# Kernel optimization log

Hardware: AMD Instinct MI355X
Metric: run time of the kernel (lower is better)

The kernel has to match this reference:

```python
import jax, jax.numpy as jnp
import numpy as np

THRESHOLD = 0.5
ALPHA = 1.0
RATIO = 1.0
BACKGROUND = 0
OBJECT = 1


def cxcywh_to_xyxy(b):
    cxcy, wh = b[..., :2], b[..., 2:]
    return jnp.concatenate([cxcy - wh / 2.0, cxcy + wh / 2.0], axis=-1)


def xyxy_to_cxcywh(b):
    xy1, xy2 = b[..., :2], b[..., 2:]
    return jnp.concatenate([(xy1 + xy2) / 2.0, xy2 - xy1], axis=-1)


def cxcywh_to_gcxgcy(c, d):
    # standard SSD encoding with variances (0.1, 0.2)
    g_cxcy = (c[..., :2] - d[..., :2]) / (d[..., 2:] / 10.0)
    g_wh = jnp.log(c[..., 2:] / d[..., 2:]) * 5.0
    return jnp.concatenate([g_cxcy, g_wh], axis=-1)


def box_iou(a, b):
    # a: [M,4] xyxy, b: [A,4] xyxy -> [M,A]
    area_a = (a[:, 2] - a[:, 0]) * (a[:, 3] - a[:, 1])
    area_b = (b[:, 2] - b[:, 0]) * (b[:, 3] - b[:, 1])
    lt = jnp.maximum(a[:, None, :2], b[None, :, :2])
    rb = jnp.minimum(a[:, None, 2:], b[None, :, 2:])
    wh = jnp.clip(rb - lt, 0.0)
    inter = wh[..., 0] * wh[..., 1]
    return inter / (area_a[:, None] + area_b[None, :] - inter)


def setup_inputs() -> dict:
    B, A, M = 32, 16384, 64
    key = jax.random.key(0)
    k1, k2, k3, k4 = jax.random.split(key, 4)
    x = jax.random.normal(k1, (B, A, 4), dtype=jnp.float32)
    y = jax.random.normal(k2, (B, A, 2), dtype=jnp.float32)
    # valid xyxy GT boxes in [0,1]
    u = jax.random.uniform(k3, (B, M, 4), dtype=jnp.float32)
    xy1 = u[..., :2] * 0.7
    wh = 0.05 + u[..., 2:] * 0.25
    boxes = jnp.concatenate([xy1, xy1 + wh], axis=-1)
    # default (prior) boxes in cxcywh
    ud = jax.random.uniform(k4, (A, 4), dtype=jnp.float32)
    dcxcy = 0.05 + ud[..., :2] * 0.9
    dwh = 0.05 + ud[..., 2:] * 0.25
    default = jnp.concatenate([dcxcy, dwh], axis=-1)
    labels = jnp.ones((B, M), dtype=jnp.int32)  # all GT boxes are 'object'
    return {"x": x, "y": y, "boxes": boxes, "labels": labels, "default": default}


def reference(x, y, boxes, labels, default):
    B, A = x.shape[0], default.shape[0]
    M = boxes.shape[1]
    default_xy = cxcywh_to_xyxy(default)  # [A,4]

    def match(bx):  # bx: [M,4]
        iou = box_iou(bx, default_xy)              # [M,A]
        overlap = iou.max(axis=0)                  # [A] best GT per anchor
        digit = jnp.argmax(iou, axis=0)            # [A]
        best_anchor = jnp.argmax(iou, axis=1)      # [M] best anchor per GT
        digit = digit.at[best_anchor].set(jnp.arange(M))
        overlap = overlap.at[best_anchor].set(1.0)
        return digit, overlap

    digit, overlap = jax.vmap(match)(boxes)        # [B,A], [B,A]
    matched = jnp.take_along_axis(boxes, digit[..., None], axis=1)  # [B,A,4]
    localization = cxcywh_to_gcxgcy(xyxy_to_cxcywh(matched), default)  # [B,A,4]

    gathered = jnp.take_along_axis(labels, digit, axis=1)           # [B,A]
    classification = jnp.where(overlap < THRESHOLD, BACKGROUND, gathered)

    positives = classification == OBJECT
    total = positives.sum()
    totf = total.astype(x.dtype)

    # SmoothL1 (beta=1), mean over positive elements (P*4)
    d = x - localization
    ad = jnp.abs(d)
    sl1 = jnp.where(ad < 1.0, 0.5 * d * d, ad - 0.5)
    smooth = (sl1 * positives[..., None]).sum() / (totf * 4.0)

    # per-anchor cross entropy
    logp = jax.nn.log_softmax(y, axis=-1)                 # [B,A,2]
    ent = -jnp.take_along_axis(logp, classification[..., None], axis=-1)[..., 0]

    pos_sum = jnp.where(positives, ent, 0.0).sum()
    # hard negative mining: sort negatives descending, keep int(total*ratio)
    negv = jnp.where(positives, 0.0, ent).ravel()         # CE >= 0, so masking with 0 is safe
    neg_sorted = jnp.sort(negv)[::-1]
    keep = (totf * RATIO).astype(jnp.int32)
    neg_sum = jnp.where(jnp.arange(negv.shape[0]) < keep, neg_sorted, 0.0).sum()

    entropy = ALPHA * (pos_sum + neg_sum) / totf
    return smooth + entropy
```

## Files before the change

kernel.cpp:

```cpp
#include <hip/hip_runtime.h>

#define THRESH 0.5f

__global__ void __launch_bounds__(256) k_matchboth(
        const float* __restrict__ boxes, const float* __restrict__ dflt,
        unsigned* __restrict__ match, unsigned long long* __restrict__ bestchunk,
        unsigned* __restrict__ zerop, int B, int A, int M, int chunks) {
    __shared__ float4 bx[128];
    __shared__ float barea[128];
    __shared__ float4 anch[256];
    __shared__ float adarea[256];
    __shared__ unsigned long long lm[128];
    int tid = threadIdx.x;
    if (blockIdx.x == 0) {
        for (int j = tid; j < 4112; j += 256) zerop[j] = 0u;
    }
    int b = blockIdx.x / chunks;
    int chunk = blockIdx.x - b * chunks;
    int a = chunk * 256 + tid;
    if (tid < M) {
        float4 bv = *reinterpret_cast<const float4*>(boxes + ((size_t)b * M + tid) * 4);
        bx[tid] = bv;
        barea[tid] = (bv.z - bv.x) * (bv.w - bv.y);
        lm[tid] = 0ull;
    }
    bool aval = (a < A);
    float dx1 = 0.f, dy1 = 0.f, dx2 = 0.f, dy2 = 0.f, darea = 0.f;
    if (aval) {
        float4 dv = *reinterpret_cast<const float4*>(dflt + (size_t)a * 4);
        dx1 = dv.x - dv.z * 0.5f; dy1 = dv.y - dv.w * 0.5f;
        dx2 = dv.x + dv.z * 0.5f; dy2 = dv.y + dv.w * 0.5f;
        darea = (dx2 - dx1) * (dy2 - dy1);
    }
    anch[tid] = make_float4(dx1, dy1, dx2, dy2);
    adarea[tid] = darea;
    __syncthreads();
    if (aval) {
        float binter = -1.0f, bS = 1.0f; int bm = 0;
        #pragma unroll 4
        for (int m = 0; m < M; ++m) {
            float4 bb = bx[m];
            float lx = fmaxf(bb.x, dx1), ly = fmaxf(bb.y, dy1);
            float rx = fminf(bb.z, dx2), ry = fminf(bb.w, dy2);
            float w = fmaxf(rx - lx, 0.f), h = fmaxf(ry - ly, 0.f);
            float inter = w * h;
            float S = barea[m] + darea;
            bool gt = inter * bS > binter * S;
            binter = gt ? inter : binter;
            bS     = gt ? S : bS;
            bm     = gt ? m : bm;
        }
        unsigned fl = (3.0f * binter >= bS) ? (1u << 30) : 0u;
        match[(size_t)b * A + a] = (unsigned)bm | fl;
    }
    int wv = tid >> 6, lane = tid & 63;
    int abase = chunk * 256 + wv * 64;
    int kmax = min(64, A - abase);
    if (lane < M && kmax > 0) {
        float4 bb = bx[lane];
        float ba = barea[lane];
        float binter = -1.0f, bS = 1.0f; int bk = 0;
        #pragma unroll 4
        for (int k = 0; k < kmax; ++k) {
            float4 av = anch[wv * 64 + k];
            float lx = fmaxf(bb.x, av.x), ly = fmaxf(bb.y, av.y);
            float rx = fminf(bb.z, av.z), ry = fminf(bb.w, av.w);
            float w = fmaxf(rx - lx, 0.f), h = fmaxf(ry - ly, 0.f);
            float inter = w * h;
            float S = ba + adarea[wv * 64 + k];
            bool gt = inter * bS > binter * S;
            binter = gt ? inter : binter;
            bS     = gt ? S : bS;
            bk     = gt ? k : bk;
        }
        float best = binter / (bS - binter);
        atomicMax(&lm[lane], ((unsigned long long)__float_as_uint(best) << 32) |
                             (unsigned long long)(unsigned)(~(abase + bk)));
    }
    __syncthreads();
    if (tid < M)
        bestchunk[((size_t)b * chunks + chunk) * M + tid] = lm[tid];
}

__global__ void __launch_bounds__(256) k_main(
        const float* __restrict__ x, const float* __restrict__ y,
        const float* __restrict__ boxes, const int* __restrict__ labels,
        const float* __restrict__ dflt, const unsigned* __restrict__ match,
        const unsigned long long* __restrict__ bestchunk,
        float* __restrict__ negv, unsigned* __restrict__ hist1,
        unsigned* __restrict__ scal, int A, int M, int chunks, int N) {
    __shared__ unsigned lh[2048];
    __shared__ float4 sbx[128];
    __shared__ int slab[128];
    __shared__ int ovr[1024];
    int tid = threadIdx.x;
    for (int j = tid; j < 2048; j += 256) lh[j] = 0u;
    for (int j = tid; j < 1024; j += 256) ovr[j] = -1;
    int i0 = (blockIdx.x * 256 + tid) * 4;
    int base = blockIdx.x * 1024;
    int b = (int)(((long long)blockIdx.x * 1024) / A);
    if (tid < M) {
        sbx[tid] = *reinterpret_cast<const float4*>(boxes + ((size_t)b * M + tid) * 4);
        slab[tid] = labels[b * M + tid];
    }
    __syncthreads();
    if (tid < M) {
        unsigned long long p = 0ull;
        const unsigned long long* bp = bestchunk + (size_t)b * chunks * M + tid;
        for (int c = 0; c < chunks; ++c) {
            unsigned long long q = bp[(size_t)c * M];
            p = (q > p) ? q : p;
        }
        unsigned a = ~(unsigned)(p & 0xFFFFFFFFull);
        int target = b * A + (int)a;
        if (target >= base && target < base + 1024)
            atomicMax(&ovr[target - base], tid);
    }
    __syncthreads();
    float l_smooth = 0.f, l_pos = 0.f; int l_cnt = 0;
    if (i0 + 3 < N) {
        uint4 w4 = *reinterpret_cast<const uint4*>(match + i0);
        const float4* yp = reinterpret_cast<const float4*>(y + (size_t)i0 * 2);
        float4 ya = yp[0], yb = yp[1];
        unsigned wws[4] = {w4.x, w4.y, w4.z, w4.w};
        float y0s[4] = {ya.x, ya.z, yb.x, yb.z};
        float y1s[4] = {ya.y, ya.w, yb.y, yb.w};
        float vs[4];
        int a0 = i0 - b * A;
        #pragma unroll
        for (int e = 0; e < 4; ++e) {
            unsigned w = wws[e];
            int digit = (int)(w & 0xFFFFu);
            bool flag = (w & 0x40000000u) != 0u;
            int o = ovr[tid * 4 + e];
            if (o >= 0) { digit = o; flag = true; }
            int c = flag ? slab[digit] : 0;
            bool pos = (c == 1);
            float y0 = y0s[e], y1v = y1s[e];
            float mx = fmaxf(y0, y1v);
            float lse = mx + log1pf(expf(-fabsf(y0 - y1v)));
            float ent = lse - ((c == 0) ? y0 : y1v);
            float v = pos ? 0.f : ent;
            vs[e] = v;
            if (pos) {
                float4 bv = sbx[digit];
                float4 dv = *reinterpret_cast<const float4*>(dflt + (size_t)(a0 + e) * 4);
                float4 xv = *reinterpret_cast<const float4*>(x + (size_t)(i0 + e) * 4);
                float cw = bv.z - bv.x, ch = bv.w - bv.y;
                float ccx = (bv.x + bv.z) * 0.5f, ccy = (bv.y + bv.w) * 0.5f;
                float l0 = (ccx - dv.x) / (dv.z * 0.1f);
                float l1 = (ccy - dv.y) / (dv.w * 0.1f);
                float l2 = logf(cw / dv.z) * 5.f;
                float l3 = logf(ch / dv.w) * 5.f;
                float s = 0.f, d, ad;
                d = xv.x - l0; ad = fabsf(d); s += (ad < 1.f) ? 0.5f * d * d : ad - 0.5f;
                d = xv.y - l1; ad = fabsf(d); s += (ad < 1.f) ? 0.5f * d * d : ad - 0.5f;
                d = xv.z - l2; ad = fabsf(d); s += (ad < 1.f) ? 0.5f * d * d : ad - 0.5f;
                d = xv.w - l3; ad = fabsf(d); s += (ad < 1.f) ? 0.5f * d * d : ad - 0.5f;
                l_smooth += s; l_pos += ent; l_cnt += 1;
            }
            atomicAdd(&lh[__float_as_uint(v) >> 21], 1u);
        }
        *reinterpret_cast<float4*>(negv + i0) = make_float4(vs[0], vs[1], vs[2], vs[3]);
    }
    for (int off = 32; off > 0; off >>= 1) {
        l_smooth += __shfl_down(l_smooth, off, 64);
        l_pos    += __shfl_down(l_pos, off, 64);
        l_cnt    += __shfl_down(l_cnt, off, 64);
    }
    __shared__ float rs[4], rp[4]; __shared__ int rc[4];
    int wv = tid >> 6;
    if ((tid & 63) == 0) { rs[wv] = l_smooth; rp[wv] = l_pos; rc[wv] = l_cnt; }
    __syncthreads();
    if (tid == 0) {
        float ss = rs[0] + rs[1] + rs[2] + rs[3];
        float pp = rp[0] + rp[1] + rp[2] + rp[3];
        int   cc = rc[0] + rc[1] + rc[2] + rc[3];
        if (ss != 0.f) atomicAdd((float*)&scal[2], ss);
        if (pp != 0.f) atomicAdd((float*)&scal[1], pp);
        if (cc)        atomicAdd((int*)&scal[0], cc);
    }
    __syncthreads();
    for (int j = tid; j < 2048; j += 256) {
        unsigned h = lh[j];
        if (h) atomicAdd(&hist1[j], h);
    }
}

__device__ __forceinline__ void scan_find(const unsigned* __restrict__ hist, int nbins,
                                          unsigned k, unsigned* ts, unsigned* res) {
    int t = threadIdx.x;
    int per = nbins >> 8;
    unsigned s = 0;
    for (int j = 0; j < per; ++j) s += hist[t * per + j];
    ts[t] = s;
    __syncthreads();
    for (int off = 1; off < 256; off <<= 1) {
        unsigned add = (t >= off) ? ts[t - off] : 0u;
        __syncthreads();
        ts[t] += add;
        __syncthreads();
    }
    unsigned total = ts[255];
    unsigned P = (t == 0) ? 0u : ts[t - 1];
    for (int j = 0; j < per; ++j) {
        unsigned h = hist[t * per + j];
        P += h;
        unsigned above = total - P;
        if (above < k && k <= above + h) { res[0] = (unsigned)(t * per + j); res[1] = k - above; }
    }
    __syncthreads();
}

__global__ void __launch_bounds__(256) k_refine2(
        const float* __restrict__ negv, int N, const unsigned* __restrict__ scal,
        const unsigned* __restrict__ hist1, unsigned* __restrict__ hist2) {
    __shared__ unsigned ts[256], res[2], lh[2048];
    scan_find(hist1, 2048, scal[0], ts, res);
    unsigned bin1 = res[0];
    for (int j = threadIdx.x; j < 2048; j += 256) lh[j] = 0u;
    __syncthreads();
    for (int i = (blockIdx.x * 256 + threadIdx.x) * 4; i < N; i += gridDim.x * 1024) {
        float4 v4 = *reinterpret_cast<const float4*>(negv + i);
        unsigned u;
        u = __float_as_uint(v4.x); if ((u >> 21) == bin1) atomicAdd(&lh[(u >> 10) & 0x7FFu], 1u);
        u = __float_as_uint(v4.y); if ((u >> 21) == bin1) atomicAdd(&lh[(u >> 10) & 0x7FFu], 1u);
        u = __float_as_uint(v4.z); if ((u >> 21) == bin1) atomicAdd(&lh[(u >> 10) & 0x7FFu], 1u);
        u = __float_as_uint(v4.w); if ((u >> 21) == bin1) atomicAdd(&lh[(u >> 10) & 0x7FFu], 1u);
    }
    __syncthreads();
    for (int j = threadIdx.x; j < 2048; j += 256) {
        unsigned h = lh[j];
        if (h) atomicAdd(&hist2[j], h);
    }
}

__global__ void __launch_bounds__(256) k_sum(
        const float* __restrict__ negv, int N, unsigned* __restrict__ scal,
        const unsigned* __restrict__ hist1, const unsigned* __restrict__ hist2,
        float* __restrict__ out) {
    __shared__ unsigned ts[256], res[2];
    scan_find(hist1, 2048, scal[0], ts, res);
    unsigned bin1 = res[0], k1 = res[1];
    scan_find(hist2, 2048, k1, ts, res);
    unsigned bin2 = res[0], k2 = res[1];
    unsigned tb = (bin1 << 21) | (bin2 << 10) | 0x3FFu;
    float s = 0.f;
    for (int i = (blockIdx.x * 256 + threadIdx.x) * 4; i < N; i += gridDim.x * 1024) {
        float4 v4 = *reinterpret_cast<const float4*>(negv + i);
        unsigned u;
        u = __float_as_uint(v4.x); if (u > tb) s += v4.x;
        u = __float_as_uint(v4.y); if (u > tb) s += v4.y;
        u = __float_as_uint(v4.z); if (u > tb) s += v4.z;
        u = __float_as_uint(v4.w); if (u > tb) s += v4.w;
    }
    for (int off = 32; off > 0; off >>= 1) s += __shfl_down(s, off, 64);
    __shared__ float rsum[4];
    __shared__ unsigned isLast;
    int wv = threadIdx.x >> 6;
    if ((threadIdx.x & 63) == 0) rsum[wv] = s;
    __syncthreads();
    if (threadIdx.x == 0) {
        float ss = rsum[0] + rsum[1] + rsum[2] + rsum[3];
        if (ss != 0.f) atomicAdd((float*)&scal[9], ss);
        __threadfence();
        unsigned prev = atomicAdd(&scal[12], 1u);
        isLast = (prev == gridDim.x - 1) ? 1u : 0u;
    }
    __syncthreads();
    if (isLast && threadIdx.x == 0) {
        __threadfence();
        volatile unsigned* vs = scal;
        volatile float* vf = (volatile float*)scal;
        float k = (float)vs[0];
        float tmid = __uint_as_float((bin1 << 21) | (bin2 << 10) | 512u);
        float neg_sum = vf[9] + (float)k2 * tmid;
        float smooth = vf[2] / (k * 4.f);
        float ent = (vf[1] + neg_sum) / k;
        out[0] = smooth + ent;
    }
}

extern "C" void kernel_launch(void* const* d_in, const int* in_sizes, int n_in,
                              void* d_out, int out_size, void* d_ws, size_t ws_size,
                              hipStream_t stream) {
    const float* x      = (const float*)d_in[0];
    const float* y      = (const float*)d_in[1];
    const float* boxes  = (const float*)d_in[2];
    const int*   labels = (const int*)d_in[3];
    const float* dflt   = (const float*)d_in[4];
    float* out = (float*)d_out;

    int A = in_sizes[4] / 4;
    int B = in_sizes[1] / (2 * A);
    int M = in_sizes[3] / B;
    int N = B * A;
    int chunks = (A + 255) / 256;

    unsigned* ws    = (unsigned*)d_ws;
    unsigned* match = ws;
    float*    negv  = (float*)(ws + (size_t)N);
    unsigned long long* bestchunk = (unsigned long long*)(ws + (size_t)2 * N);
    unsigned* hist1 = ws + (size_t)2 * N + (size_t)2 * B * chunks * M;
    unsigned* hist2 = hist1 + 2048;
    unsigned* scal  = hist2 + 2048;

    k_matchboth<<<dim3(B * chunks), dim3(256), 0, stream>>>(boxes, dflt, match, bestchunk,
                                                            hist1, B, A, M, chunks);
    k_main<<<dim3(N / 1024), dim3(256), 0, stream>>>(x, y, boxes, labels, dflt, match, bestchunk,
                                                     negv, hist1, scal, A, M, chunks, N);
    k_refine2<<<dim3(256), dim3(256), 0, stream>>>(negv, N, scal, hist1, hist2);
    k_sum<<<dim3(256), dim3(256), 0, stream>>>(negv, N, scal, hist1, hist2, out);
}
```

Before: 153.9 us.

## Move best-anchor override to tiny kernel and fuse refine/sum passes over negatives

The per-GT best-anchor override is now computed once by a small kernel that atomically patches the match array. Before, every k_main block reduced all bestchunk entries for its image into shared memory before doing its own work. The second histogram pass and the final threshold sum are merged into one pass. That pass accumulates per-sub-bin counts and value sums, and the last block resolves the second-level threshold. This removes one full read of the negatives array and the redundant per-block reductions, at the cost of an extra launch and float atomics into shared memory.

New measurement: 161.7 us. 5.1% more time.

```diff
diff --git a/kernel.cpp b/kernel.cpp
--- a/kernel.cpp
+++ b/kernel.cpp
@@ -13,7 +13,7 @@
     __shared__ unsigned long long lm[128];
     int tid = threadIdx.x;
     if (blockIdx.x == 0) {
-        for (int j = tid; j < 4112; j += 256) zerop[j] = 0u;
+        for (int j = tid; j < 6160; j += 256) zerop[j] = 0u;
     }
     int b = blockIdx.x / chunks;
     int chunk = blockIdx.x - b * chunks;
@@ -82,46 +82,45 @@
         bestchunk[((size_t)b * chunks + chunk) * M + tid] = lm[tid];
 }
 
+__global__ void k_override(const unsigned long long* __restrict__ bestchunk,
+                           unsigned* __restrict__ match, int B, int A, int M, int chunks) {
+    int i = blockIdx.x * blockDim.x + threadIdx.x;
+    if (i >= B * M) return;
+    int b = i / M, m = i - b * M;
+    const unsigned long long* bp = bestchunk + (size_t)b * chunks * M + m;
+    unsigned long long p = 0ull;
+    for (int c = 0; c < chunks; ++c) {
+        unsigned long long q = bp[(size_t)c * M];
+        p = (q > p) ? q : p;
+    }
+    unsigned a = ~(unsigned)(p & 0xFFFFFFFFull);
+    if (a < (unsigned)A)
+        atomicMax(&match[(size_t)b * A + a], 0x80000000u | (unsigned)m);
+}
+
 __global__ void __launch_bounds__(256) k_main(
         const float* __restrict__ x, const float* __restrict__ y,
         const float* __restrict__ boxes, const int* __restrict__ labels,
         const float* __restrict__ dflt, const unsigned* __restrict__ match,
-        const unsigned long long* __restrict__ bestchunk,
         float* __restrict__ negv, unsigned* __restrict__ hist1,
-        unsigned* __restrict__ scal, int A, int M, int chunks, int N) {
+        unsigned* __restrict__ scal, int A, int M, int N) {
     __shared__ unsigned lh[2048];
     __shared__ float4 sbx[128];
     __shared__ int slab[128];
-    __shared__ int ovr[1024];
     int tid = threadIdx.x;
+    int i0 = (blockIdx.x * 256 + tid) * 4;
+    int b = (int)(((long long)blockIdx.x * 1024) / A);
+    uint4 w4 = *reinterpret_cast<const uint4*>(match + i0);
+    const float4* yp = reinterpret_cast<const float4*>(y + (size_t)i0 * 2);
+    float4 ya = yp[0], yb = yp[1];
     for (int j = tid; j < 2048; j += 256) lh[j] = 0u;
-    for (int j = tid; j < 1024; j += 256) ovr[j] = -1;
-    int i0 = (blockIdx.x * 256 + tid) * 4;
-    int base = blockIdx.x * 1024;
-    int b = (int)(((long long)blockIdx.x * 1024) / A);
     if (tid < M) {
         sbx[tid] = *reinterpret_cast<const float4*>(boxes + ((size_t)b * M + tid) * 4);
         slab[tid] = labels[b * M + tid];
     }
     __syncthreads();
-    if (tid < M) {
-        unsigned long long p = 0ull;
-        const unsigned long long* bp = bestchunk + (size_t)b * chunks * M + tid;
-        for (int c = 0; c < chunks; ++c) {
-            unsigned long long q = bp[(size_t)c * M];
-            p = (q > p) ? q : p;
-        }
-        unsigned a = ~(unsigned)(p & 0xFFFFFFFFull);
-        int target = b * A + (int)a;
-        if (target >= base && target < base + 1024)
-            atomicMax(&ovr[target - base], tid);
-    }
-    __syncthreads();
     float l_smooth = 0.f, l_pos = 0.f; int l_cnt = 0;
-    if (i0 + 3 < N) {
-        uint4 w4 = *reinterpret_cast<const uint4*>(match + i0);
-        const float4* yp = reinterpret_cast<const float4*>(y + (size_t)i0 * 2);
-        float4 ya = yp[0], yb = yp[1];
+    {
         unsigned wws[4] = {w4.x, w4.y, w4.z, w4.w};
         float y0s[4] = {ya.x, ya.z, yb.x, yb.z};
         float y1s[4] = {ya.y, ya.w, yb.y, yb.w};
@@ -131,9 +130,7 @@
         for (int e = 0; e < 4; ++e) {
             unsigned w = wws[e];
             int digit = (int)(w & 0xFFFFu);
-            bool flag = (w & 0x40000000u) != 0u;
-            int o = ovr[tid * 4 + e];
-            if (o >= 0) { digit = o; flag = true; }
+            bool flag = (w & 0xC0000000u) != 0u;
             int c = flag ? slab[digit] : 0;
             bool pos = (c == 1);
             float y0 = y0s[e], y1v = y1s[e];
@@ -187,7 +184,7 @@
     }
 }
 
-__device__ __forceinline__ void scan_find(const unsigned* __restrict__ hist, int nbins,
+__device__ __forceinline__ void scan_find(const unsigned* hist, int nbins,
                                           unsigned k, unsigned* ts, unsigned* res) {
     int t = threadIdx.x;
     int per = nbins >> 8;
@@ -213,54 +210,46 @@
 }
 
 __global__ void __launch_bounds__(256) k_refine2(
-        const float* __restrict__ negv, int N, const unsigned* __restrict__ scal,
-        const unsigned* __restrict__ hist1, unsigned* __restrict__ hist2) {
-    __shared__ unsigned ts[256], res[2], lh[2048];
-    scan_find(hist1, 2048, scal[0], ts, res);
-    unsigned bin1 = res[0];
-    for (int j = threadIdx.x; j < 2048; j += 256) lh[j] = 0u;
-    __syncthreads();
-    for (int i = (blockIdx.x * 256 + threadIdx.x) * 4; i < N; i += gridDim.x * 1024) {
-        float4 v4 = *reinterpret_cast<const float4*>(negv + i);
-        unsigned u;
-        u = __float_as_uint(v4.x); if ((u >> 21) == bin1) atomicAdd(&lh[(u >> 10) & 0x7FFu], 1u);
-        u = __float_as_uint(v4.y); if ((u >> 21) == bin1) atomicAdd(&lh[(u >> 10) & 0x7FFu], 1u);
-        u = __float_as_uint(v4.z); if ((u >> 21) == bin1) atomicAdd(&lh[(u >> 10) & 0x7FFu], 1u);
-        u = __float_as_uint(v4.w); if ((u >> 21) == bin1) atomicAdd(&lh[(u >> 10) & 0x7FFu], 1u);
-    }
-    __syncthreads();
-    for (int j = threadIdx.x; j < 2048; j += 256) {
-        unsigned h = lh[j];
-        if (h) atomicAdd(&hist2[j], h);
-    }
-}
-
-__global__ void __launch_bounds__(256) k_sum(
         const float* __restrict__ negv, int N, unsigned* __restrict__ scal,
-        const unsigned* __restrict__ hist1, const unsigned* __restrict__ hist2,
-        float* __restrict__ out) {
+        const unsigned* __restrict__ hist1, unsigned* __restrict__ hist2,
+        float* __restrict__ fsum2, float* __restrict__ out) {
     __shared__ unsigned ts[256], res[2];
+    __shared__ unsigned lh[2048];
+    __shared__ float lf[2048];
+    int tid = threadIdx.x;
     scan_find(hist1, 2048, scal[0], ts, res);
     unsigned bin1 = res[0], k1 = res[1];
-    scan_find(hist2, 2048, k1, ts, res);
-    unsigned bin2 = res[0], k2 = res[1];
-    unsigned tb = (bin1 << 21) | (bin2 << 10) | 0x3FFu;
-    float s = 0.f;
-    for (int i = (blockIdx.x * 256 + threadIdx.x) * 4; i < N; i += gridDim.x * 1024) {
+    for (int j = tid; j < 2048; j += 256) { lh[j] = 0u; lf[j] = 0.f; }
+    __syncthreads();
+    float sacc = 0.f;
+    int i = (blockIdx.x * 256 + tid) * 4;
+    if (i + 3 < N) {
         float4 v4 = *reinterpret_cast<const float4*>(negv + i);
-        unsigned u;
-        u = __float_as_uint(v4.x); if (u > tb) s += v4.x;
-        u = __float_as_uint(v4.y); if (u > tb) s += v4.y;
-        u = __float_as_uint(v4.z); if (u > tb) s += v4.z;
-        u = __float_as_uint(v4.w); if (u > tb) s += v4.w;
-    }
-    for (int off = 32; off > 0; off >>= 1) s += __shfl_down(s, off, 64);
+        float vv[4] = {v4.x, v4.y, v4.z, v4.w};
+        #pragma unroll
+        for (int e = 0; e < 4; ++e) {
+            unsigned u = __float_as_uint(vv[e]);
+            unsigned b1 = u >> 21;
+            if (b1 > bin1) sacc += vv[e];
+            else if (b1 == bin1) {
+                unsigned j = (u >> 10) & 0x7FFu;
+                atomicAdd(&lh[j], 1u);
+                atomicAdd(&lf[j], vv[e]);
+            }
+        }
+    }
+    __syncthreads();
+    for (int j = tid; j < 2048; j += 256) {
+        unsigned h = lh[j];
+        if (h) { atomicAdd(&hist2[j], h); atomicAdd(&fsum2[j], lf[j]); }
+    }
+    for (int off = 32; off > 0; off >>= 1) sacc += __shfl_down(sacc, off, 64);
     __shared__ float rsum[4];
     __shared__ unsigned isLast;
-    int wv = threadIdx.x >> 6;
-    if ((threadIdx.x & 63) == 0) rsum[wv] = s;
-    __syncthreads();
-    if (threadIdx.x == 0) {
+    int wv = tid >> 6;
+    if ((tid & 63) == 0) rsum[wv] = sacc;
+    __syncthreads();
+    if (tid == 0) {
         float ss = rsum[0] + rsum[1] + rsum[2] + rsum[3];
         if (ss != 0.f) atomicAdd((float*)&scal[9], ss);
         __threadfence();
@@ -268,13 +257,27 @@
         isLast = (prev == gridDim.x - 1) ? 1u : 0u;
     }
     __syncthreads();
-    if (isLast && threadIdx.x == 0) {
-        __threadfence();
+    if (!isLast) return;
+    for (int j = tid; j < 2048; j += 256) {
+        lh[j] = ((volatile unsigned*)hist2)[j];
+        lf[j] = ((volatile float*)fsum2)[j];
+    }
+    __syncthreads();
+    scan_find(lh, 2048, k1, ts, res);
+    unsigned bin2 = res[0], k2 = res[1];
+    float fs = 0.f;
+    for (int j = tid; j < 2048; j += 256)
+        if (j > (int)bin2) fs += lf[j];
+    for (int off = 32; off > 0; off >>= 1) fs += __shfl_down(fs, off, 64);
+    if ((tid & 63) == 0) rsum[wv] = fs;
+    __syncthreads();
+    if (tid == 0) {
+        float fst = rsum[0] + rsum[1] + rsum[2] + rsum[3];
         volatile unsigned* vs = scal;
         volatile float* vf = (volatile float*)scal;
         float k = (float)vs[0];
         float tmid = __uint_as_float((bin1 << 21) | (bin2 << 10) | 512u);
-        float neg_sum = vf[9] + (float)k2 * tmid;
+        float neg_sum = vf[9] + fst + (float)k2 * tmid;
         float smooth = vf[2] / (k * 4.f);
         float ent = (vf[1] + neg_sum) / k;
         out[0] = smooth + ent;
@@ -303,12 +306,13 @@
     unsigned long long* bestchunk = (unsigned long long*)(ws + (size_t)2 * N);
     unsigned* hist1 = ws + (size_t)2 * N + (size_t)2 * B * chunks * M;
     unsigned* hist2 = hist1 + 2048;
-    unsigned* scal  = hist2 + 2048;
+    float*    fsum2 = (float*)(hist2 + 2048);
+    unsigned* scal  = (unsigned*)(fsum2 + 2048);
 
     k_matchboth<<<dim3(B * chunks), dim3(256), 0, stream>>>(boxes, dflt, match, bestchunk,
                                                             hist1, B, A, M, chunks);
-    k_main<<<dim3(N / 1024), dim3(256), 0, stream>>>(x, y, boxes, labels, dflt, match, bestchunk,
-                                                     negv, hist1, scal, A, M, chunks, N);
-    k_refine2<<<dim3(256), dim3(256), 0, stream>>>(negv, N, scal, hist1, hist2);
-    k_sum<<<dim3(256), dim3(256), 0, stream>>>(negv, N, scal, hist1, hist2, out);
-}
+    k_override<<<dim3((B * M + 255) / 256), dim3(256), 0, stream>>>(bestchunk, match, B, A, M, chunks);
+    k_main<<<dim3(N / 1024), dim3(256), 0, stream>>>(x, y, boxes, labels, dflt, match,
+                                                     negv, hist1, scal, A, M, N);
+    k_refine2<<<dim3(N / 1024), dim3(256), 0, stream>>>(negv, N, scal, hist1, hist2, fsum2, out);
+}
```
